# Optimization experiments

Hardware: AMD Instinct MI355X
Metric: run time of the kernel (lower is better)

The kernel has to match this reference:

```python
import jax, jax.numpy as jnp
import numpy as np

PS = 16
E = 512          # embed_dim
H = 8            # num_heads
EPS = 1e-5


def _ln(x, g, b):
    m = jnp.mean(x, axis=-1, keepdims=True)
    v = jnp.mean((x - m) ** 2, axis=-1, keepdims=True)
    return (x - m) * jax.lax.rsqrt(v + EPS) * g + b


def _mha(q_in, kv_in, in_w, in_b, out_w, out_b):
    # torch nn.MultiheadAttention: packed in_proj [3E, E], out_proj [E, E]
    Bq, Lq, _ = q_in.shape
    Lk = kv_in.shape[1]
    d = E // H
    wq, wk, wv = jnp.split(in_w, 3, axis=0)
    bq, bk, bv = jnp.split(in_b, 3, axis=0)
    q = (q_in @ wq.T + bq).reshape(Bq, Lq, H, d)
    k = (kv_in @ wk.T + bk).reshape(Bq, Lk, H, d)
    v = (kv_in @ wv.T + bv).reshape(Bq, Lk, H, d)
    scores = jnp.einsum('bqhd,bkhd->bhqk', q, k) / jnp.sqrt(jnp.float32(d))
    a = jax.nn.softmax(scores, axis=-1)
    o = jnp.einsum('bhqk,bkhd->bqhd', a, v).reshape(Bq, Lq, E)
    return o @ out_w.T + out_b


def setup_inputs() -> dict:
    key = jax.random.key(0)
    ks = jax.random.split(key, 24)
    s = 0.02
    D = 3 * PS * PS
    inp = {
        'neighbor_patches': jax.random.normal(ks[0], (8, 32, 32, 9, 3, PS, PS), jnp.float32),
        'w_pe': jax.random.normal(ks[1], (E, D), jnp.float32) * s,
        'b_pe': jnp.zeros((E,), jnp.float32),
        'pos_embed': jax.random.normal(ks[2], (1, 9, E), jnp.float32),
        'sa_in_w': jax.random.normal(ks[3], (3 * E, E), jnp.float32) * s,
        'sa_in_b': jnp.zeros((3 * E,), jnp.float32),
        'sa_out_w': jax.random.normal(ks[4], (E, E), jnp.float32) * s,
        'sa_out_b': jnp.zeros((E,), jnp.float32),
        'g1': jnp.ones((E,), jnp.float32), 'beta1': jnp.zeros((E,), jnp.float32),
        'ca_in_w': jax.random.normal(ks[5], (3 * E, E), jnp.float32) * s,
        'ca_in_b': jnp.zeros((3 * E,), jnp.float32),
        'ca_out_w': jax.random.normal(ks[6], (E, E), jnp.float32) * s,
        'ca_out_b': jnp.zeros((E,), jnp.float32),
        'g2': jnp.ones((E,), jnp.float32), 'beta2': jnp.zeros((E,), jnp.float32),
        'w1': jax.random.normal(ks[7], (4 * E, E), jnp.float32) * s,
        'b1': jnp.zeros((4 * E,), jnp.float32),
        'w2': jax.random.normal(ks[8], (E, 4 * E), jnp.float32) * s,
        'b2': jnp.zeros((E,), jnp.float32),
        'g3': jnp.ones((E,), jnp.float32), 'beta3': jnp.zeros((E,), jnp.float32),
    }
    return inp


def reference(neighbor_patches, w_pe, b_pe, pos_embed,
              sa_in_w, sa_in_b, sa_out_w, sa_out_b, g1, beta1,
              ca_in_w, ca_in_b, ca_out_w, ca_out_b, g2, beta2,
              w1, b1, w2, b2, g3, beta3):
    B, NH, NW, NN, C, ps, _ = neighbor_patches.shape
    x = neighbor_patches.reshape(B * NH * NW, NN, C * ps * ps)
    x = x @ w_pe.T + b_pe                       # [BN, 9, E]
    x = x + pos_embed
    attn = _mha(x, x, sa_in_w, sa_in_b, sa_out_w, sa_out_b)
    x = _ln(x + attn, g1, beta1)
    cq = x[:, 4:5, :]                            # center query [BN, 1, E]
    attn = _mha(cq, x, ca_in_w, ca_in_b, ca_out_w, ca_out_b)
    c = _ln(cq + attn, g2, beta2)
    ffn = jax.nn.gelu(c @ w1.T + b1, approximate=False) @ w2.T + b2
    out = _ln(c + ffn, g3, beta3)
    return out[:, 0, :].reshape(B, NH * NW, E)
```

## Files before the change

### kernel.cpp

```cpp
#include <hip/hip_runtime.h>


typedef unsigned short u16;
typedef u16   u16x8 __attribute__((ext_vector_type(8)));
typedef u16   u16x4 __attribute__((ext_vector_type(4)));
typedef __bf16 bf16x8 __attribute__((ext_vector_type(8)));
typedef __bf16 bf16x4 __attribute__((ext_vector_type(4)));
typedef float f32x4 __attribute__((ext_vector_type(4)));

static __device__ __forceinline__ u16 f2bf(float f) {
  union { float f; unsigned u; } v; v.f = f;
  unsigned r = v.u + 0x7FFFu + ((v.u >> 16) & 1u);
  return (u16)(r >> 16);
}
static __device__ __forceinline__ float bf2f(u16 u) {
  union { unsigned u; float f; } v; v.u = ((unsigned)u) << 16;
  return v.f;
}

static __device__ __forceinline__ void gld16(const void* g, void* l) {
  __builtin_amdgcn_global_load_lds(
      (__attribute__((address_space(1))) unsigned int*)(size_t)g,
      (__attribute__((address_space(3))) unsigned int*)(unsigned)(size_t)l,
      16, 0, 0);
}

static __device__ __forceinline__ int xcd_swz(int bid, int nwg) {
  int q = nwg >> 3, r = nwg & 7;
  int xcd = bid & 7, sub = bid >> 3;
  return (xcd < r ? xcd * (q + 1) : r * (q + 1) + (xcd - r) * q) + sub;
}

#define BAR   __builtin_amdgcn_s_barrier()
#define VM0   asm volatile("s_waitcnt vmcnt(0)" ::: "memory")
#define VM4   asm volatile("s_waitcnt vmcnt(4)" ::: "memory")
#define VM6   asm volatile("s_waitcnt vmcnt(6)" ::: "memory")
#define LGKM0 asm volatile("s_waitcnt lgkmcnt(0)" ::: "memory")

__global__ __launch_bounds__(256, 3) void gemm_pe(
    const float* __restrict__ A, int lda,
    const u16* __restrict__ W,
    const float* __restrict__ bias,
    const float* __restrict__ pos,
    u16* out, int M, int N, int K, int nbx)
{
  __shared__ u16 As[2][4096];
  __shared__ u16 Bs[2][4096];

  const int t    = threadIdx.x;
  const int lane = t & 63, wv = t >> 6;
  const int swz  = xcd_swz(blockIdx.x, gridDim.x);
  const int bm   = (swz / nbx) * 128, bn = (swz % nbx) * 128;
  const int wr   = wv >> 1, wc = wv & 1;

  const int srow = lane >> 2;
  const int skk  = (((lane & 3) ^ ((lane >> 3) & 3)) << 3);
  const int lr = lane & 15;
  const int rg = (((lane >> 4) ^ ((lr >> 1) & 3)) << 3);

  f32x4 acc[4][4] = {};
  float4 areg0[4], areg1[4];

  auto stageB = [&](int buf, int kt) {
    #pragma unroll
    for (int c = 0; c < 2; ++c) {
      int rr = (wv + 4 * c) * 16 + srow;
      gld16(W + (size_t)(bn + rr) * K + kt * 32 + skk, &Bs[buf][(wv + 4 * c) * 512]);
    }
  };
  auto loadA = [&](float4 (&dst)[4], int kt) {
    #pragma unroll
    for (int i = 0; i < 4; ++i) {
      int idx = i * 256 + t, r = idx >> 3, c4 = (idx & 7) * 4;
      dst[i] = *(const float4*)(A + (size_t)(bm + r) * lda + kt * 32 + c4);
    }
  };
  auto writeA = [&](int buf, float4 (&src)[4]) {
    #pragma unroll
    for (int i = 0; i < 4; ++i) {
      int idx = i * 256 + t, r = idx >> 3, c4 = (idx & 7) * 4;
      int g = (c4 >> 3) ^ ((r >> 1) & 3);
      int off = r * 32 + g * 8 + (c4 & 4);
      bf16x4 h;
      h.x = (__bf16)src[i].x; h.y = (__bf16)src[i].y;
      h.z = (__bf16)src[i].z; h.w = (__bf16)src[i].w;
      *(u16x4*)&As[buf][off] = *(u16x4*)&h;
    }
  };
  auto mfma_on = [&](int cur) {
    bf16x8 a[4], b[4];
    #pragma unroll
    for (int m = 0; m < 4; ++m)
      a[m] = *(const bf16x8*)&As[cur][(wr * 64 + m * 16 + lr) * 32 + rg];
    #pragma unroll
    for (int n = 0; n < 4; ++n)
      b[n] = *(const bf16x8*)&Bs[cur][(wc * 64 + n * 16 + lr) * 32 + rg];
    #pragma unroll
    for (int m = 0; m < 4; ++m)
      #pragma unroll
      for (int n = 0; n < 4; ++n)
        acc[m][n] = __builtin_amdgcn_mfma_f32_16x16x32_bf16(a[m], b[n], acc[m][n], 0, 0, 0);
  };

  const int nkt = K >> 5;
  loadA(areg0, 0);
  stageB(0, 0);
  loadA(areg1, 1);
  VM6;
  writeA(0, areg0);
  VM4;
  LGKM0; BAR;

  auto iter = [&](int kt, float4 (&wset)[4], float4 (&lset)[4]) {
    const bool pf1 = kt + 1 < nkt, pf2 = kt + 2 < nkt;
    const int cur = kt & 1;
    if (pf1) {
      VM0;
      writeA(cur ^ 1, wset);
      stageB(cur ^ 1, kt + 1);
    }
    if (pf2) loadA(lset, kt + 2);
    mfma_on(cur);
    if (pf1) { if (pf2) { VM4; } else { VM0; } }
    LGKM0; BAR;
  };
  for (int kt = 0; kt < nkt; kt += 2) {
    iter(kt,     areg1, areg0);
    iter(kt + 1, areg0, areg1);
  }

  const int lq = lane >> 4;
  #pragma unroll
  for (int m = 0; m < 4; ++m) {
    #pragma unroll
    for (int n = 0; n < 4; ++n) {
      int col = bn + wc * 64 + n * 16 + lr;
      float bv = bias[col];
      #pragma unroll
      for (int r = 0; r < 4; ++r) {
        int row = bm + wr * 64 + m * 16 + lq * 4 + r;
        float v = acc[m][n][r] + bv + pos[(row % 9) * 512 + col];
        out[(size_t)row * N + col] = f2bf(v);
      }
    }
  }
}

template<bool HAS_RES, bool HAS_GELU>
__global__ __launch_bounds__(512, 4) void gemm_t(
    const u16* __restrict__ A, int lda,
    const u16* __restrict__ W,
    const float* __restrict__ bias,
    const u16* res, int res_stride,
    u16* out,
    int M, int N, int K, int nbx)
{
  __shared__ u16 As[2][8192];
  __shared__ u16 Bs[2][4096];

  const int t    = threadIdx.x;
  const int lane = t & 63, wv = t >> 6;
  const int swz  = xcd_swz(blockIdx.x, gridDim.x);
  const int bm   = (swz / nbx) * 256, bn = (swz % nbx) * 128;
  const int wr   = wv >> 1, wc = wv & 1;

  const int srow = lane >> 2;
  const int skk  = (((lane & 3) ^ ((lane >> 3) & 3)) << 3);
  const int lr = lane & 15;
  const int rg = (((lane >> 4) ^ ((lr >> 1) & 3)) << 3);

  f32x4 acc[4][4] = {};

  auto stage = [&](int buf, int kt) {
    #pragma unroll
    for (int c = 0; c < 2; ++c) {
      int rr = wv * 32 + c * 16 + srow;
      gld16(A + (size_t)(bm + rr) * lda + kt * 32 + skk,
            &As[buf][(wv * 2 + c) * 512]);
    }
    int rb = wv * 16 + srow;
    gld16(W + (size_t)(bn + rb) * K + kt * 32 + skk, &Bs[buf][wv * 512]);
  };

  const int nkt = K >> 5;
  stage(0, 0);
  VM0; BAR;

  int cur = 0;
  for (int kt = 0; kt < nkt; ++kt) {
    const bool pf = (kt + 1 < nkt);
    if (pf) stage(cur ^ 1, kt + 1);

    bf16x8 a[4], b[4];
    #pragma unroll
    for (int m = 0; m < 4; ++m)
      a[m] = *(const bf16x8*)&As[cur][(wr * 64 + m * 16 + lr) * 32 + rg];
    #pragma unroll
    for (int n = 0; n < 4; ++n)
      b[n] = *(const bf16x8*)&Bs[cur][(wc * 64 + n * 16 + lr) * 32 + rg];
    #pragma unroll
    for (int m = 0; m < 4; ++m)
      #pragma unroll
      for (int n = 0; n < 4; ++n)
        acc[m][n] = __builtin_amdgcn_mfma_f32_16x16x32_bf16(a[m], b[n], acc[m][n], 0, 0, 0);

    if (pf) VM0;
    BAR;
    cur ^= 1;
  }

  const int lq = lane >> 4;
  #pragma unroll
  for (int m = 0; m < 4; ++m) {
    #pragma unroll
    for (int n = 0; n < 4; ++n) {
      int col = bn + wc * 64 + n * 16 + lr;
      float bv = bias[col];
      #pragma unroll
      for (int r = 0; r < 4; ++r) {
        int row = bm + wr * 64 + m * 16 + lq * 4 + r;
        float v = acc[m][n][r] + bv;
        if constexpr (HAS_RES) v += bf2f(res[(size_t)row * res_stride + col]);
        if constexpr (HAS_GELU) v = 0.5f * v * (1.f + erff(v * 0.70710678118f));
        out[(size_t)row * N + col] = f2bf(v);
      }
    }
  }
}

template<bool HAS_RES, bool HAS_GELU>
__global__ __launch_bounds__(256, 6) void gemm_s(
    const u16* __restrict__ A, int lda,
    const u16* __restrict__ W,
    const float* __restrict__ bias,
    const u16* res, int res_stride,
    u16* out,
    int M, int N, int K, int nbx)
{
  __shared__ u16 As[2][2048];
  __shared__ u16 Bs[2][4096];

  const int t    = threadIdx.x;
  const int lane = t & 63, wv = t >> 6;
  const int swz  = xcd_swz(blockIdx.x, gridDim.x);
  const int bm   = (swz / nbx) * 64, bn = (swz % nbx) * 128;
  const int wc   = wv;

  const int srow = lane >> 2;
  const int skk  = (((lane & 3) ^ ((lane >> 3) & 3)) << 3);
  const int lr = lane & 15;
  const int rg = (((lane >> 4) ^ ((lr >> 1) & 3)) << 3);

  f32x4 acc[4][2] = {};

  auto stage = [&](int buf, int kt) {
    gld16(A + (size_t)(bm + wv * 16 + srow) * lda + kt * 32 + skk,
          &As[buf][wv * 512]);
    #pragma unroll
    for (int c = 0; c < 2; ++c) {
      int rr = (wv + 4 * c) * 16 + srow;
      gld16(W + (size_t)(bn + rr) * K + kt * 32 + skk, &Bs[buf][(wv + 4 * c) * 512]);
    }
  };

  const int nkt = K >> 5;
  stage(0, 0);
  VM0; BAR;

  int cur = 0;
  for (int kt = 0; kt < nkt; ++kt) {
    const bool pf = (kt + 1 < nkt);
    if (pf) stage(cur ^ 1, kt + 1);

    bf16x8 a[4], b[2];
    #pragma unroll
    for (int m = 0; m < 4; ++m)
      a[m] = *(const bf16x8*)&As[cur][(m * 16 + lr) * 32 + rg];
    #pragma unroll
    for (int n = 0; n < 2; ++n)
      b[n] = *(const bf16x8*)&Bs[cur][(wc * 32 + n * 16 + lr) * 32 + rg];
    #pragma unroll
    for (int m = 0; m < 4; ++m)
      #pragma unroll
      for (int n = 0; n < 2; ++n)
        acc[m][n] = __builtin_amdgcn_mfma_f32_16x16x32_bf16(a[m], b[n], acc[m][n], 0, 0, 0);

    if (pf) VM0;
    BAR;
    cur ^= 1;
  }

  const int lq = lane >> 4;
  #pragma unroll
  for (int m = 0; m < 4; ++m) {
    #pragma unroll
    for (int n = 0; n < 2; ++n) {
      int col = bn + wc * 32 + n * 16 + lr;
      float bv = bias[col];
      #pragma unroll
      for (int r = 0; r < 4; ++r) {
        int row = bm + m * 16 + lq * 4 + r;
        float v = acc[m][n][r] + bv;
        if constexpr (HAS_RES) v += bf2f(res[(size_t)row * res_stride + col]);
        if constexpr (HAS_GELU) v = 0.5f * v * (1.f + erff(v * 0.70710678118f));
        out[(size_t)row * N + col] = f2bf(v);
      }
    }
  }
}

__global__ __launch_bounds__(256) void ln_k(
    const u16* in,
    const float* __restrict__ g, const float* __restrict__ be,
    u16* out_bf, float* out_f32, int rows)
{
  int wv = threadIdx.x >> 6, lane = threadIdx.x & 63;
  int row = blockIdx.x * 4 + wv;
  if (row >= rows) return;
  const u16* p = in + (size_t)row * 512;
  u16x8 v = *(const u16x8*)&p[lane * 8];
  float x[8], s = 0.f, sq = 0.f;
  #pragma unroll
  for (int j = 0; j < 8; ++j) { x[j] = bf2f(v[j]); s += x[j]; sq += x[j] * x[j]; }
  #pragma unroll
  for (int o = 32; o > 0; o >>= 1) { s += __shfl_xor(s, o, 64); sq += __shfl_xor(sq, o, 64); }
  float mean = s * (1.f / 512.f);
  float var  = sq * (1.f / 512.f) - mean * mean;
  float rs   = rsqrtf(var + 1e-5f);
  float y[8];
  #pragma unroll
  for (int j = 0; j < 8; ++j) {
    int c = lane * 8 + j;
    y[j] = (x[j] - mean) * rs * g[c] + be[c];
  }
  if (out_bf) {
    u16x8 o8;
    #pragma unroll
    for (int j = 0; j < 8; ++j) o8[j] = f2bf(y[j]);
    *(u16x8*)&out_bf[(size_t)row * 512 + lane * 8] = o8;
  }
  if (out_f32) {
    #pragma unroll
    for (int j = 0; j < 8; ++j) out_f32[(size_t)row * 512 + lane * 8 + j] = y[j];
  }
}

__global__ __launch_bounds__(256) void sa_attn_k(const u16* __restrict__ qkv,
                                                 u16* __restrict__ out)
{
  __shared__ u16  s_qkv[9 * 1536];
  __shared__ float s_sc[8][81];
  const int s = blockIdx.x, t = threadIdx.x;
  const u16* src = qkv + (size_t)s * 9 * 1536;
  for (int i = t; i < (9 * 1536) / 8; i += 256)
    *(u16x8*)&s_qkv[i * 8] = *(const u16x8*)&src[i * 8];
  __syncthreads();

  const int h = t >> 5, sl = t & 31;
  for (int p = sl; p < 81; p += 32) {
    int qi = p / 9, ki = p % 9;
    const u16* qp = &s_qkv[qi * 1536 + h * 64];
    const u16* kp = &s_qkv[ki * 1536 + 512 + h * 64];
    float d = 0.f;
    #pragma unroll
    for (int e8 = 0; e8 < 8; ++e8) {
      u16x8 qv = *(const u16x8*)&qp[e8 * 8];
      u16x8 kv = *(const u16x8*)&kp[e8 * 8];
      #pragma unroll
      for (int j = 0; j < 8; ++j) d += bf2f(qv[j]) * bf2f(kv[j]);
    }
    s_sc[h][p] = d * 0.125f;
  }
  __syncthreads();

  if (t < 72) {
    int hh = t / 9, qi = t % 9;
    float* sc = &s_sc[hh][qi * 9];
    float mx = sc[0];
    #pragma unroll
    for (int i = 1; i < 9; ++i) mx = fmaxf(mx, sc[i]);
    float e[9], sum = 0.f;
    #pragma unroll
    for (int i = 0; i < 9; ++i) { e[i] = __expf(sc[i] - mx); sum += e[i]; }
    float inv = 1.f / sum;
    #pragma unroll
    for (int i = 0; i < 9; ++i) sc[i] = e[i] * inv;
  }
  __syncthreads();

  for (int gidx = sl; gidx < 72; gidx += 32) {
    int qi = gidx >> 3, dg = gidx & 7;
    float a[8] = {};
    #pragma unroll
    for (int ki = 0; ki < 9; ++ki) {
      float pr = s_sc[h][qi * 9 + ki];
      u16x8 vv = *(const u16x8*)&s_qkv[ki * 1536 + 1024 + h * 64 + dg * 8];
      #pragma unroll
      for (int j = 0; j < 8; ++j) a[j] += pr * bf2f(vv[j]);
    }
    u16x8 o8;
    #pragma unroll
    for (int j = 0; j < 8; ++j) o8[j] = f2bf(a[j]);
    *(u16x8*)&out[((size_t)s * 9 + qi) * 512 + h * 64 + dg * 8] = o8;
  }
}

__global__ __launch_bounds__(256) void ca_attn_k(const u16* __restrict__ q,
                                                 const u16* __restrict__ kv,
                                                 u16* __restrict__ out)
{
  __shared__ u16  s_q[512];
  __shared__ u16  s_kv[9 * 1024];
  __shared__ float s_sc[8][9];
  const int s = blockIdx.x, t = threadIdx.x;
  if (t < 64) *(u16x8*)&s_q[t * 8] = *(const u16x8*)&q[(size_t)s * 512 + t * 8];
  for (int i = t; i < (9 * 1024) / 8; i += 256)
    *(u16x8*)&s_kv[i * 8] = *(const u16x8*)&kv[(size_t)s * 9 * 1024 + i * 8];
  __syncthreads();

  if (t < 72) {
    int h = t / 9, ki = t % 9;
    const u16* qp = &s_q[h * 64];
    const u16* kp = &s_kv[ki * 1024 + h * 64];
    float d = 0.f;
    #pragma unroll
    for (int e8 = 0; e8 < 8; ++e8) {
      u16x8 qv = *(const u16x8*)&qp[e8 * 8];
      u16x8 kvv = *(const u16x8*)&kp[e8 * 8];
      #pragma unroll
      for (int j = 0; j < 8; ++j) d += bf2f(qv[j]) * bf2f(kvv[j]);
    }
    s_sc[h][ki] = d * 0.125f;
  }
  __syncthreads();

  if (t < 8) {
    float* sc = s_sc[t];
    float mx = sc[0];
    #pragma unroll
    for (int i = 1; i < 9; ++i) mx = fmaxf(mx, sc[i]);
    float e[9], sum = 0.f;
    #pragma unroll
    for (int i = 0; i < 9; ++i) { e[i] = __expf(sc[i] - mx); sum += e[i]; }
    float inv = 1.f / sum;
    #pragma unroll
    for (int i = 0; i < 9; ++i) sc[i] = e[i] * inv;
  }
  __syncthreads();

  if (t < 64) {
    int h = t >> 3, dg = t & 7;
    float a[8] = {};
    #pragma unroll
    for (int ki = 0; ki < 9; ++ki) {
      float pr = s_sc[h][ki];
      u16x8 vv = *(const u16x8*)&s_kv[ki * 1024 + 512 + h * 64 + dg * 8];
      #pragma unroll
      for (int j = 0; j < 8; ++j) a[j] += pr * bf2f(vv[j]);
    }
    u16x8 o8;
    #pragma unroll
    for (int j = 0; j < 8; ++j) o8[j] = f2bf(a[j]);
    *(u16x8*)&out[(size_t)s * 512 + h * 64 + dg * 8] = o8;
  }
}

__global__ __launch_bounds__(256) void wcvt_k(
    const float* s0, const float* s1, const float* s2, const float* s3,
    const float* s4, const float* s5, const float* s6, u16* dst)
{
  int b = blockIdx.x;
  const float* sp; long base, segStart;
  if      (b < 384)  { sp = s0; base = 0;       segStart = 0;    }
  else if (b < 1152) { sp = s1; base = 393216;  segStart = 384;  }
  else if (b < 1408) { sp = s2; base = 1179648; segStart = 1152; }
  else if (b < 2176) { sp = s3; base = 1441792; segStart = 1408; }
  else if (b < 2432) { sp = s4; base = 2228224; segStart = 2176; }
  else if (b < 3456) { sp = s5; base = 2490368; segStart = 2432; }
  else               { sp = s6; base = 3538944; segStart = 3456; }
  long loc = ((long)b - segStart) * 1024 + (long)threadIdx.x * 4;
  float4 f = *(const float4*)(sp + loc);
  u16x4 o; o.x = f2bf(f.x); o.y = f2bf(f.y); o.z = f2bf(f.z); o.w = f2bf(f.w);
  *(u16x4*)&dst[base + loc] = o;
}

extern "C" void kernel_launch(void* const* d_in, const int* in_sizes, int n_in,
                              void* d_out, int out_size, void* d_ws, size_t ws_size,
                              hipStream_t stream)
{
  const float* patches  = (const float*)d_in[0];
  const float* w_pe     = (const float*)d_in[1];
  const float* b_pe     = (const float*)d_in[2];
  const float* pos      = (const float*)d_in[3];
  const float* sa_in_w  = (const float*)d_in[4];
  const float* sa_in_b  = (const float*)d_in[5];
  const float* sa_out_w = (const float*)d_in[6];
  const float* sa_out_b = (const float*)d_in[7];
  const float* g1       = (const float*)d_in[8];
  const float* beta1    = (const float*)d_in[9];
  const float* ca_in_w  = (const float*)d_in[10];
  const float* ca_in_b  = (const float*)d_in[11];
  const float* ca_out_w = (const float*)d_in[12];
  const float* ca_out_b = (const float*)d_in[13];
  const float* g2       = (const float*)d_in[14];
  const float* beta2    = (const float*)d_in[15];
  const float* w1       = (const float*)d_in[16];
  const float* b1       = (const float*)d_in[17];
  const float* w2       = (const float*)d_in[18];
  const float* b2       = (const float*)d_in[19];
  const float* g3       = (const float*)d_in[20];
  const float* beta3    = (const float*)d_in[21];
  float* out = (float*)d_out;

  char* base = (char*)d_ws;
  u16* wbf        = (u16*)base;
  u16* w_pe_bf    = wbf;
  u16* sa_in_bf   = wbf + 393216;
  u16* sa_out_bf  = wbf + 1179648;
  u16* ca_in_bf   = wbf + 1441792;
  u16* ca_out_bf  = wbf + 2228224;
  u16* w1_bf      = wbf + 2490368;
  u16* w2_bf      = wbf + 3538944;
  u16* x_bf  = (u16*)(base + 9175040ull);
  u16* qkv   = (u16*)(base + 84672512ull);
  u16* sattn = (u16*)(base + 311164928ull);
  u16* q_bf  = (u16*)(base + 386662400ull);
  u16* cattn = (u16*)(base + 395051008ull);
  u16* csum  = (u16*)(base + 403439616ull);
  u16* h_bf  = (u16*)(base + 411828224ull);
  u16* osum  = (u16*)(base + 445382656ull);

  wcvt_k<<<4480, 256, 0, stream>>>(w_pe, sa_in_w, sa_out_w, ca_in_w,
                                   ca_out_w, w1, w2, wbf);

  gemm_pe<<<2304, 256, 0, stream>>>(
      patches, 768, w_pe_bf, b_pe, pos, x_bf, 73728, 512, 768, 4);
  gemm_t<false, false><<<3456, 512, 0, stream>>>(
      x_bf, 512, sa_in_bf, sa_in_b, nullptr, 0, qkv, 73728, 1536, 512, 12);
  sa_attn_k<<<8192, 256, 0, stream>>>(qkv, sattn);
  gemm_t<true, false><<<1152, 512, 0, stream>>>(
      sattn, 512, sa_out_bf, sa_out_b, x_bf, 512, x_bf, 73728, 512, 512, 4);
  ln_k<<<73728 / 4, 256, 0, stream>>>(x_bf, g1, beta1, x_bf, nullptr, 73728);
  gemm_s<false, false><<<512, 256, 0, stream>>>(
      x_bf + 2048, 4608, ca_in_bf, ca_in_b, nullptr, 0, q_bf, 8192, 512, 512, 4);
  gemm_t<false, false><<<2304, 512, 0, stream>>>(
      x_bf, 512, ca_in_bf + 262144, ca_in_b + 512, nullptr, 0, qkv, 73728, 1024, 512, 8);
  ca_attn_k<<<8192, 256, 0, stream>>>(q_bf, qkv, cattn);
  gemm_s<true, false><<<512, 256, 0, stream>>>(
      cattn, 512, ca_out_bf, ca_out_b, x_bf + 2048, 4608, csum, 8192, 512, 512, 4);
  ln_k<<<8192 / 4, 256, 0, stream>>>(csum, g2, beta2, csum, nullptr, 8192);
  gemm_t<false, true><<<512, 512, 0, stream>>>(
      csum, 512, w1_bf, b1, nullptr, 0, h_bf, 8192, 2048, 512, 16);
  gemm_s<true, false><<<512, 256, 0, stream>>>(
      h_bf, 2048, w2_bf, b2, csum, 512, osum, 8192, 512, 2048, 4);
  ln_k<<<8192 / 4, 256, 0, stream>>>(osum, g3, beta3, nullptr, out, 8192);
}
```

Baseline: 753.4 us.

## Use 256x256 tile, 1024-thread GEMM for patch-embed and large projection GEMMs

Replaces the 128x128 patch-embedding GEMM and the 128x256 gemm_t used for the self-attention QKV and cross-attention KV projections with one templated 256x256-tile kernel of 16 waves. The templates cover an fp32 A input converted to bf16 in registers, or a bf16 A staged directly into LDS, with an optional positional-embedding add. Larger tiles raise operand reuse and cut the block count. The kernel uses a simpler single-stage prefetch and waits on all outstanding loads every k-step. This may expose more load latency, and 1024-thread blocks with 64KB LDS limit occupancy.

```diff
diff --git a/kernel.cpp b/kernel.cpp
--- a/kernel.cpp
+++ b/kernel.cpp
@@ -33,25 +33,25 @@
 
 #define BAR   __builtin_amdgcn_s_barrier()
 #define VM0   asm volatile("s_waitcnt vmcnt(0)" ::: "memory")
-#define VM4   asm volatile("s_waitcnt vmcnt(4)" ::: "memory")
-#define VM6   asm volatile("s_waitcnt vmcnt(6)" ::: "memory")
 #define LGKM0 asm volatile("s_waitcnt lgkmcnt(0)" ::: "memory")
 
-__global__ __launch_bounds__(256, 3) void gemm_pe(
-    const float* __restrict__ A, int lda,
+template<bool A_F32, bool HAS_POS>
+__global__ __launch_bounds__(1024, 4) void gemm_q(
+    const void* Av, int lda,
     const u16* __restrict__ W,
     const float* __restrict__ bias,
     const float* __restrict__ pos,
-    u16* out, int M, int N, int K, int nbx)
-{
-  __shared__ u16 As[2][4096];
-  __shared__ u16 Bs[2][4096];
+    u16* out,
+    int M, int N, int K, int nbx)
+{
+  __shared__ u16 As[2][8192];
+  __shared__ u16 Bs[2][8192];
 
   const int t    = threadIdx.x;
   const int lane = t & 63, wv = t >> 6;
   const int swz  = xcd_swz(blockIdx.x, gridDim.x);
-  const int bm   = (swz / nbx) * 128, bn = (swz % nbx) * 128;
-  const int wr   = wv >> 1, wc = wv & 1;
+  const int bm   = (swz / nbx) * 256, bn = (swz % nbx) * 256;
+  const int wr   = wv >> 2, wc = wv & 3;
 
   const int srow = lane >> 2;
   const int skk  = (((lane & 3) ^ ((lane >> 3) & 3)) << 3);
@@ -59,35 +59,56 @@
   const int rg = (((lane >> 4) ^ ((lr >> 1) & 3)) << 3);
 
   f32x4 acc[4][4] = {};
-  float4 areg0[4], areg1[4];
-
+  float4 areg[2];
+
+  auto stageA16 = [&](int buf, int kt) {
+    const u16* A = (const u16*)Av;
+    gld16(A + (size_t)(bm + wv * 16 + srow) * lda + kt * 32 + skk,
+          &As[buf][wv * 512]);
+  };
   auto stageB = [&](int buf, int kt) {
-    #pragma unroll
-    for (int c = 0; c < 2; ++c) {
-      int rr = (wv + 4 * c) * 16 + srow;
-      gld16(W + (size_t)(bn + rr) * K + kt * 32 + skk, &Bs[buf][(wv + 4 * c) * 512]);
-    }
+    gld16(W + (size_t)(bn + wv * 16 + srow) * K + kt * 32 + skk,
+          &Bs[buf][wv * 512]);
   };
-  auto loadA = [&](float4 (&dst)[4], int kt) {
-    #pragma unroll
-    for (int i = 0; i < 4; ++i) {
-      int idx = i * 256 + t, r = idx >> 3, c4 = (idx & 7) * 4;
-      dst[i] = *(const float4*)(A + (size_t)(bm + r) * lda + kt * 32 + c4);
+  auto loadA = [&](int kt) {
+    const float* A = (const float*)Av;
+    #pragma unroll
+    for (int i = 0; i < 2; ++i) {
+      int idx = i * 1024 + t, r = idx >> 3, c4 = (idx & 7) * 4;
+      areg[i] = *(const float4*)(A + (size_t)(bm + r) * lda + kt * 32 + c4);
     }
   };
-  auto writeA = [&](int buf, float4 (&src)[4]) {
-    #pragma unroll
-    for (int i = 0; i < 4; ++i) {
-      int idx = i * 256 + t, r = idx >> 3, c4 = (idx & 7) * 4;
+  auto writeA = [&](int buf) {
+    #pragma unroll
+    for (int i = 0; i < 2; ++i) {
+      int idx = i * 1024 + t, r = idx >> 3, c4 = (idx & 7) * 4;
       int g = (c4 >> 3) ^ ((r >> 1) & 3);
       int off = r * 32 + g * 8 + (c4 & 4);
       bf16x4 h;
-      h.x = (__bf16)src[i].x; h.y = (__bf16)src[i].y;
-      h.z = (__bf16)src[i].z; h.w = (__bf16)src[i].w;
+      h.x = (__bf16)areg[i].x; h.y = (__bf16)areg[i].y;
+      h.z = (__bf16)areg[i].z; h.w = (__bf16)areg[i].w;
       *(u16x4*)&As[buf][off] = *(u16x4*)&h;
     }
   };
-  auto mfma_on = [&](int cur) {
+
+  const int nkt = K >> 5;
+  if constexpr (A_F32) {
+    loadA(0); stageB(0, 0);
+    VM0; writeA(0);
+    LGKM0; BAR;
+  } else {
+    stageA16(0, 0); stageB(0, 0);
+    VM0; BAR;
+  }
+
+  int cur = 0;
+  for (int kt = 0; kt < nkt; ++kt) {
+    const bool pf = (kt + 1 < nkt);
+    if (pf) {
+      if constexpr (A_F32) { loadA(kt + 1); stageB(cur ^ 1, kt + 1); }
+      else                 { stageA16(cur ^ 1, kt + 1); stageB(cur ^ 1, kt + 1); }
+    }
+
     bf16x8 a[4], b[4];
     #pragma unroll
     for (int m = 0; m < 4; ++m)
@@ -100,33 +121,13 @@
       #pragma unroll
       for (int n = 0; n < 4; ++n)
         acc[m][n] = __builtin_amdgcn_mfma_f32_16x16x32_bf16(a[m], b[n], acc[m][n], 0, 0, 0);
-  };
-
-  const int nkt = K >> 5;
-  loadA(areg0, 0);
-  stageB(0, 0);
-  loadA(areg1, 1);
-  VM6;
-  writeA(0, areg0);
-  VM4;
-  LGKM0; BAR;
-
-  auto iter = [&](int kt, float4 (&wset)[4], float4 (&lset)[4]) {
-    const bool pf1 = kt + 1 < nkt, pf2 = kt + 2 < nkt;
-    const int cur = kt & 1;
-    if (pf1) {
+
+    if (pf) {
       VM0;
-      writeA(cur ^ 1, wset);
-      stageB(cur ^ 1, kt + 1);
-    }
-    if (pf2) loadA(lset, kt + 2);
-    mfma_on(cur);
-    if (pf1) { if (pf2) { VM4; } else { VM0; } }
-    LGKM0; BAR;
-  };
-  for (int kt = 0; kt < nkt; kt += 2) {
-    iter(kt,     areg1, areg0);
-    iter(kt + 1, areg0, areg1);
+      if constexpr (A_F32) { writeA(cur ^ 1); LGKM0; }
+    }
+    BAR;
+    cur ^= 1;
   }
 
   const int lq = lane >> 4;
@@ -139,7 +140,8 @@
       #pragma unroll
       for (int r = 0; r < 4; ++r) {
         int row = bm + wr * 64 + m * 16 + lq * 4 + r;
-        float v = acc[m][n][r] + bv + pos[(row % 9) * 512 + col];
+        float v = acc[m][n][r] + bv;
+        if constexpr (HAS_POS) v += pos[(row % 9) * 512 + col];
         out[(size_t)row * N + col] = f2bf(v);
       }
     }
@@ -533,18 +535,18 @@
   wcvt_k<<<4480, 256, 0, stream>>>(w_pe, sa_in_w, sa_out_w, ca_in_w,
                                    ca_out_w, w1, w2, wbf);
 
-  gemm_pe<<<2304, 256, 0, stream>>>(
-      patches, 768, w_pe_bf, b_pe, pos, x_bf, 73728, 512, 768, 4);
-  gemm_t<false, false><<<3456, 512, 0, stream>>>(
-      x_bf, 512, sa_in_bf, sa_in_b, nullptr, 0, qkv, 73728, 1536, 512, 12);
+  gemm_q<true, true><<<576, 1024, 0, stream>>>(
+      patches, 768, w_pe_bf, b_pe, pos, x_bf, 73728, 512, 768, 2);
+  gemm_q<false, false><<<1728, 1024, 0, stream>>>(
+      x_bf, 512, sa_in_bf, sa_in_b, nullptr, qkv, 73728, 1536, 512, 6);
   sa_attn_k<<<8192, 256, 0, stream>>>(qkv, sattn);
   gemm_t<true, false><<<1152, 512, 0, stream>>>(
       sattn, 512, sa_out_bf, sa_out_b, x_bf, 512, x_bf, 73728, 512, 512, 4);
   ln_k<<<73728 / 4, 256, 0, stream>>>(x_bf, g1, beta1, x_bf, nullptr, 73728);
   gemm_s<false, false><<<512, 256, 0, stream>>>(
       x_bf + 2048, 4608, ca_in_bf, ca_in_b, nullptr, 0, q_bf, 8192, 512, 512, 4);
-  gemm_t<false, false><<<2304, 512, 0, stream>>>(
-      x_bf, 512, ca_in_bf + 262144, ca_in_b + 512, nullptr, 0, qkv, 73728, 1024, 512, 8);
+  gemm_q<false, false><<<1152, 1024, 0, stream>>>(
+      x_bf, 512, ca_in_bf + 262144, ca_in_b + 512, nullptr, qkv, 73728, 1024, 512, 4);
   ca_attn_k<<<8192, 256, 0, stream>>>(q_bf, qkv, cattn);
   gemm_s<true, false><<<512, 256, 0, stream>>>(
       cattn, 512, ca_out_bf, ca_out_b, x_bf + 2048, 4608, csum, 8192, 512, 512, 4);
```

Result: slower. 787.3 us (+4.5%).

## Add 256x256 8-wave pipelined GEMM for self- and cross-attention input projections

Applied to the files above, without the earlier changes.

Adds a new gemm8 kernel that computes 256x256 output tiles with 8 waves, double-buffered LDS fed by direct global-to-LDS loads, and an interleaved schedule. The schedule splits each K step into phases that overlap prefetch loads with MFMA bursts, using barriers, sched_barrier and setprio. It replaces the previous 128-tile gemm_t for the two large QKV/KV projections. The larger tiles are meant to raise arithmetic intensity and cut global traffic per FLOP. In exchange, the kernel uses much more LDS and registers, which lowers occupancy and adds many barriers.

```diff
diff --git a/kernel.cpp b/kernel.cpp
--- a/kernel.cpp
+++ b/kernel.cpp
@@ -32,10 +32,148 @@
 }
 
 #define BAR   __builtin_amdgcn_s_barrier()
+#define SB0   __builtin_amdgcn_sched_barrier(0)
+#define PRIO1 __builtin_amdgcn_s_setprio(1)
+#define PRIO0 __builtin_amdgcn_s_setprio(0)
 #define VM0   asm volatile("s_waitcnt vmcnt(0)" ::: "memory")
+#define VM2   asm volatile("s_waitcnt vmcnt(2)" ::: "memory")
 #define VM4   asm volatile("s_waitcnt vmcnt(4)" ::: "memory")
 #define VM6   asm volatile("s_waitcnt vmcnt(6)" ::: "memory")
 #define LGKM0 asm volatile("s_waitcnt lgkmcnt(0)" ::: "memory")
+
+__global__ __launch_bounds__(512, 2) void gemm8(
+    const u16* __restrict__ A, int lda,
+    const u16* __restrict__ W,
+    const float* __restrict__ bias,
+    u16* __restrict__ out,
+    int M, int N, int K, int nbx)
+{
+  __shared__ u16 As[2][2][8192];
+  __shared__ u16 Bs[2][2][8192];
+
+  const int t    = threadIdx.x;
+  const int lane = t & 63, wv = t >> 6;
+  const int swz  = xcd_swz(blockIdx.x, gridDim.x);
+  const int bm   = (swz / nbx) * 256, bn = (swz % nbx) * 256;
+  const int wr   = wv >> 2, wc = wv & 3;
+  const int bh   = wc >> 1, bro = (wc & 1) * 64;
+
+  const int sgc = (((lane & 7) ^ (lane >> 3)) << 3);
+  const int lr = lane & 15, kq = lane >> 4;
+
+  f32x4 acc[8][4] = {};
+  bf16x8 a_lo[4][2], a_hi[4][2], b[4][2];
+
+  auto stA = [&](int d, int h, int kt) {
+    #pragma unroll
+    for (int c = 0; c < 2; ++c) {
+      int R = wv * 16 + c * 8;
+      gld16(A + (size_t)(bm + h * 128 + R + (lane >> 3)) * lda + kt * 64 + sgc,
+            &As[d][h][R * 64]);
+    }
+  };
+  auto stB = [&](int d, int h, int kt) {
+    #pragma unroll
+    for (int c = 0; c < 2; ++c) {
+      int R = wv * 16 + c * 8;
+      gld16(W + (size_t)(bn + h * 128 + R + (lane >> 3)) * K + kt * 64 + sgc,
+            &Bs[d][h][R * 64]);
+    }
+  };
+  auto rdA = [&](bf16x8 (&dst)[4][2], int d, int mbase) {
+    #pragma unroll
+    for (int m = 0; m < 4; ++m)
+      #pragma unroll
+      for (int ks = 0; ks < 2; ++ks) {
+        int r = (mbase + m) * 16 + lr;
+        dst[m][ks] = *(const bf16x8*)&As[d][wr][r * 64 + (((ks * 4 + kq) ^ (lr & 7)) << 3)];
+      }
+  };
+  auto rdB = [&](int d, int nbase) {
+    #pragma unroll
+    for (int n = 0; n < 2; ++n)
+      #pragma unroll
+      for (int ks = 0; ks < 2; ++ks) {
+        int r = bro + (nbase + n) * 16 + lr;
+        b[nbase + n][ks] = *(const bf16x8*)&Bs[d][bh][r * 64 + (((ks * 4 + kq) ^ (lr & 7)) << 3)];
+      }
+  };
+  auto mf = [&](bf16x8 (&aa)[4][2], int mbase, int nbase) {
+    #pragma unroll
+    for (int m = 0; m < 4; ++m)
+      #pragma unroll
+      for (int nn = 0; nn < 2; ++nn)
+        #pragma unroll
+        for (int ks = 0; ks < 2; ++ks)
+          acc[mbase + m][nbase + nn] = __builtin_amdgcn_mfma_f32_16x16x32_bf16(
+              aa[m][ks], b[nbase + nn][ks], acc[mbase + m][nbase + nn], 0, 0, 0);
+  };
+
+  const int nkt = K >> 6, niter = nkt >> 1;
+  stA(0, 0, 0); stA(0, 1, 0); stB(0, 0, 0); stB(0, 1, 0);
+  stB(1, 0, 1); stB(1, 1, 1); stA(1, 0, 1);
+  VM6; BAR;
+
+  for (int it = 0; it < niter; ++it) {
+    const int kt2 = 2 * it + 2, kt3 = 2 * it + 3;
+    const bool pf = (it + 1 < niter);
+    stA(1, 1, 2 * it + 1);
+    rdA(a_lo, 0, 0);
+    rdB(0, 0);
+    BAR; LGKM0; SB0;
+    PRIO1; mf(a_lo, 0, 0); PRIO0;
+    BAR;
+    rdB(0, 2);
+    BAR; LGKM0; SB0;
+    PRIO1; mf(a_lo, 0, 2); PRIO0;
+    BAR;
+    if (pf) stB(0, 0, kt2);
+    rdA(a_hi, 0, 4);
+    BAR; LGKM0; SB0;
+    PRIO1; mf(a_hi, 4, 0); PRIO0;
+    BAR;
+    if (pf) { stB(0, 1, kt2); stA(0, 0, kt2); }
+    BAR;
+    PRIO1; mf(a_hi, 4, 2); PRIO0;
+    if (pf) { VM6; } else { VM0; }
+    BAR;
+    if (pf) stA(0, 1, kt2);
+    rdA(a_lo, 1, 0);
+    rdB(1, 0);
+    BAR; LGKM0; SB0;
+    PRIO1; mf(a_lo, 0, 0); PRIO0;
+    BAR;
+    rdB(1, 2);
+    BAR; LGKM0; SB0;
+    PRIO1; mf(a_lo, 0, 2); PRIO0;
+    BAR;
+    if (pf) stB(1, 0, kt3);
+    rdA(a_hi, 1, 4);
+    BAR; LGKM0; SB0;
+    PRIO1; mf(a_hi, 4, 0); PRIO0;
+    BAR;
+    if (pf) { stB(1, 1, kt3); stA(1, 0, kt3); }
+    BAR;
+    PRIO1; mf(a_hi, 4, 2); PRIO0;
+    if (pf) { VM6; } else { VM0; }
+    BAR;
+  }
+
+  const int lq = lane >> 4;
+  #pragma unroll
+  for (int m = 0; m < 8; ++m) {
+    #pragma unroll
+    for (int n = 0; n < 4; ++n) {
+      int col = bn + wc * 64 + n * 16 + lr;
+      float bv = bias[col];
+      #pragma unroll
+      for (int r = 0; r < 4; ++r) {
+        int row = bm + wr * 128 + m * 16 + lq * 4 + r;
+        out[(size_t)row * N + col] = f2bf(acc[m][n][r] + bv);
+      }
+    }
+  }
+}
 
 __global__ __launch_bounds__(256, 3) void gemm_pe(
     const float* __restrict__ A, int lda,
@@ -535,16 +673,16 @@
 
   gemm_pe<<<2304, 256, 0, stream>>>(
       patches, 768, w_pe_bf, b_pe, pos, x_bf, 73728, 512, 768, 4);
-  gemm_t<false, false><<<3456, 512, 0, stream>>>(
-      x_bf, 512, sa_in_bf, sa_in_b, nullptr, 0, qkv, 73728, 1536, 512, 12);
+  gemm8<<<1728, 512, 0, stream>>>(
+      x_bf, 512, sa_in_bf, sa_in_b, qkv, 73728, 1536, 512, 6);
   sa_attn_k<<<8192, 256, 0, stream>>>(qkv, sattn);
   gemm_t<true, false><<<1152, 512, 0, stream>>>(
       sattn, 512, sa_out_bf, sa_out_b, x_bf, 512, x_bf, 73728, 512, 512, 4);
   ln_k<<<73728 / 4, 256, 0, stream>>>(x_bf, g1, beta1, x_bf, nullptr, 73728);
   gemm_s<false, false><<<512, 256, 0, stream>>>(
       x_bf + 2048, 4608, ca_in_bf, ca_in_b, nullptr, 0, q_bf, 8192, 512, 512, 4);
-  gemm_t<false, false><<<2304, 512, 0, stream>>>(
-      x_bf, 512, ca_in_bf + 262144, ca_in_b + 512, nullptr, 0, qkv, 73728, 1024, 512, 8);
+  gemm8<<<1152, 512, 0, stream>>>(
+      x_bf, 512, ca_in_bf + 262144, ca_in_b + 512, qkv, 73728, 1024, 512, 4);
   ca_attn_k<<<8192, 256, 0, stream>>>(q_bf, qkv, cattn);
   gemm_s<true, false><<<512, 256, 0, stream>>>(
       cattn, 512, ca_out_bf, ca_out_b, x_bf + 2048, 4608, csum, 8192, 512, 512, 4);
```

After: 764.7 us. No clear change (+1.5%).
